# Kernel tuning notes

Measured on AMD Instinct MI355X. Metric: run time of the kernel, lower is better.

The kernel has to match this reference:

```python
import jax, jax.numpy as jnp
import numpy as np

B, C, F, T = 64, 1, 128, 3000
TIME_MASK, FREQ_MASK = 30, 13


def setup_inputs() -> dict:
    key = jax.random.key(0)
    kx, kt, kf, kt0, kf0 = jax.random.split(key, 5)
    x = jax.random.normal(kx, (B, C, F, T), dtype=jnp.float32)
    t = jax.random.randint(kt, (B,), 0, TIME_MASK, dtype=jnp.int32)
    f = jax.random.randint(kf, (B,), 0, FREQ_MASK, dtype=jnp.int32)
    t0 = jax.random.randint(kt0, (B,), 0, T - TIME_MASK, dtype=jnp.int32)
    f0 = jax.random.randint(kf0, (B,), 0, F - FREQ_MASK, dtype=jnp.int32)
    return {"x": x, "t": t, "f": f, "t0": t0, "f0": f0}


def reference(x, t, f, t0, f0):
    # x: [B, 1, F, T]; per-sample zero bands on freq axis [f0, f0+f) and time axis [t0, t0+t)
    freq_idx = jnp.arange(x.shape[2], dtype=jnp.int32)  # [F]
    time_idx = jnp.arange(x.shape[3], dtype=jnp.int32)  # [T]
    # keep masks: True where value is kept (outside the zeroed band)
    keep_f = ~((freq_idx[None, :] >= f0[:, None]) & (freq_idx[None, :] < f0[:, None] + f[:, None]))  # [B, F]
    keep_t = ~((time_idx[None, :] >= t0[:, None]) & (time_idx[None, :] < t0[:, None] + t[:, None]))  # [B, T]
    keep = keep_f[:, None, :, None] & keep_t[:, None, None, :]  # [B, 1, F, T]
    return jnp.where(keep, x, jnp.zeros((), dtype=x.dtype))
```

## Files before the change

kernel.cpp:

```cpp
#include <hip/hip_runtime.h>


constexpr int B_  = 64;
constexpr int F_  = 128;
constexpr int T_  = 3000;
constexpr int T4  = T_ / 4;
constexpr int ROW4 = F_ * T4;
constexpr int TOTAL4 = B_ * ROW4;

__global__ void __launch_bounds__(256)
specaug_kernel(const float4* __restrict__ x,
               const int* __restrict__ t,
               const int* __restrict__ f,
               const int* __restrict__ t0,
               const int* __restrict__ f0,
               float4* __restrict__ out) {
    const int stride = gridDim.x * blockDim.x;
    for (int i = blockIdx.x * blockDim.x + threadIdx.x; i < TOTAL4; i += stride) {
        const int b   = i / ROW4;
        const int rem = i - b * ROW4;
        const int fr  = rem / T4;
        const int tt  = (rem - fr * T4) * 4;

        const int fb = f0[b];
        const int fe = fb + f[b];
        const int tb = t0[b];
        const int te = tb + t[b];

        float4 v = x[i];
        if (fr >= fb && fr < fe) {
            v.x = 0.f; v.y = 0.f; v.z = 0.f; v.w = 0.f;
        } else {
            if (tt + 0 >= tb && tt + 0 < te) v.x = 0.f;
            if (tt + 1 >= tb && tt + 1 < te) v.y = 0.f;
            if (tt + 2 >= tb && tt + 2 < te) v.z = 0.f;
            if (tt + 3 >= tb && tt + 3 < te) v.w = 0.f;
        }
        out[i] = v;
    }
}

extern "C" void kernel_launch(void* const* d_in, const int* in_sizes, int n_in,
                              void* d_out, int out_size, void* d_ws, size_t ws_size,
                              hipStream_t stream) {
    const float4* x = (const float4*)d_in[0];
    const int* t    = (const int*)d_in[1];
    const int* f    = (const int*)d_in[2];
    const int* t0   = (const int*)d_in[3];
    const int* f0   = (const int*)d_in[4];
    float4* out     = (float4*)d_out;

    const int block = 256;
    int grid = (TOTAL4 + block - 1) / block;
    if (grid > 2048) grid = 2048;
    specaug_kernel<<<grid, block, 0, stream>>>(x, t, f, t0, f0, out);
}
```

Measured before the change: 33.77 us.

## Map one block per frequency row, skip reads of masked rows, nontemporal stores

Replaces the grid-stride flat loop with a 2D grid where each block handles one (batch, frequency) row. This removes per-element integer division and per-element mask parameter loads. Rows inside the frequency band are written as zeros without reading the input, which saves read bandwidth. Stores use nontemporal hints to reduce cache pollution. The row length of 750 vectors leaves some threads idle in the last iteration.

```diff
diff --git a/kernel.cpp b/kernel.cpp
--- a/kernel.cpp
+++ b/kernel.cpp
@@ -1,57 +1,58 @@
 #include <hip/hip_runtime.h>
 
 
-constexpr int B_  = 64;
+typedef float v4f __attribute__((ext_vector_type(4)));
+
 constexpr int F_  = 128;
-constexpr int T_  = 3000;
-constexpr int T4  = T_ / 4;
-constexpr int ROW4 = F_ * T4;
-constexpr int TOTAL4 = B_ * ROW4;
+constexpr int T4  = 750;
 
 __global__ void __launch_bounds__(256)
-specaug_kernel(const float4* __restrict__ x,
+specaug_kernel(const v4f* __restrict__ x,
                const int* __restrict__ t,
                const int* __restrict__ f,
                const int* __restrict__ t0,
                const int* __restrict__ f0,
-               float4* __restrict__ out) {
-    const int stride = gridDim.x * blockDim.x;
-    for (int i = blockIdx.x * blockDim.x + threadIdx.x; i < TOTAL4; i += stride) {
-        const int b   = i / ROW4;
-        const int rem = i - b * ROW4;
-        const int fr  = rem / T4;
-        const int tt  = (rem - fr * T4) * 4;
+               v4f* __restrict__ out) {
+    const int fr = blockIdx.x;
+    const int b  = blockIdx.y;
 
-        const int fb = f0[b];
-        const int fe = fb + f[b];
-        const int tb = t0[b];
-        const int te = tb + t[b];
+    const int fb   = f0[b];
+    const int flen = f[b];
+    const int tb   = t0[b];
+    const int tlen = t[b];
 
-        float4 v = x[i];
-        if (fr >= fb && fr < fe) {
-            v.x = 0.f; v.y = 0.f; v.z = 0.f; v.w = 0.f;
-        } else {
-            if (tt + 0 >= tb && tt + 0 < te) v.x = 0.f;
-            if (tt + 1 >= tb && tt + 1 < te) v.y = 0.f;
-            if (tt + 2 >= tb && tt + 2 < te) v.z = 0.f;
-            if (tt + 3 >= tb && tt + 3 < te) v.w = 0.f;
+    const size_t row = (size_t)(b * F_ + fr) * T4;
+    const v4f* __restrict__ src = x + row;
+    v4f* __restrict__ dst = out + row;
+
+    if ((unsigned)(fr - fb) < (unsigned)flen) {
+        const v4f z = (v4f)(0.f);
+        for (int j = threadIdx.x; j < T4; j += 256) {
+            __builtin_nontemporal_store(z, &dst[j]);
         }
-        out[i] = v;
+    } else {
+        for (int j = threadIdx.x; j < T4; j += 256) {
+            v4f v = src[j];
+            const int tt = j * 4;
+            if ((unsigned)(tt + 0 - tb) < (unsigned)tlen) v.x = 0.f;
+            if ((unsigned)(tt + 1 - tb) < (unsigned)tlen) v.y = 0.f;
+            if ((unsigned)(tt + 2 - tb) < (unsigned)tlen) v.z = 0.f;
+            if ((unsigned)(tt + 3 - tb) < (unsigned)tlen) v.w = 0.f;
+            __builtin_nontemporal_store(v, &dst[j]);
+        }
     }
 }
 
 extern "C" void kernel_launch(void* const* d_in, const int* in_sizes, int n_in,
                               void* d_out, int out_size, void* d_ws, size_t ws_size,
                               hipStream_t stream) {
-    const float4* x = (const float4*)d_in[0];
-    const int* t    = (const int*)d_in[1];
-    const int* f    = (const int*)d_in[2];
-    const int* t0   = (const int*)d_in[3];
-    const int* f0   = (const int*)d_in[4];
-    float4* out     = (float4*)d_out;
+    const v4f* x  = (const v4f*)d_in[0];
+    const int* t  = (const int*)d_in[1];
+    const int* f  = (const int*)d_in[2];
+    const int* t0 = (const int*)d_in[3];
+    const int* f0 = (const int*)d_in[4];
+    v4f* out      = (v4f*)d_out;
 
-    const int block = 256;
-    int grid = (TOTAL4 + block - 1) / block;
-    if (grid > 2048) grid = 2048;
-    specaug_kernel<<<grid, block, 0, stream>>>(x, t, f, t0, f0, out);
+    dim3 grid(F_, 64);
+    specaug_kernel<<<grid, 256, 0, stream>>>(x, t, f, t0, f0, out);
 }
```

New measurement: 34.10 us. About the same (+1.0%).
